# Kernel optimization log

Measured on AMD Instinct MI355X. Metric: run time of the kernel, lower is better.

The kernel has to match this reference:

```python
import jax, jax.numpy as jnp
import numpy as np

N = 100000   # nodes
E = 640000   # edges
DIN = 128
DOUT = 128
BN_EPS = 1e-5


def setup_inputs() -> dict:
    key = jax.random.key(0)
    k = jax.random.split(key, 6)
    x = jax.random.normal(k[0], (N, DIN), dtype=jnp.float32)
    edge_index = jax.random.randint(k[1], (2, E), 0, N, dtype=jnp.int64)
    # MLP params: Linear(DIN,DOUT) -> BatchNorm1d(DOUT) -> ReLU -> Linear(DOUT,DOUT)
    s1 = 1.0 / np.sqrt(DIN)
    s2 = 1.0 / np.sqrt(DOUT)
    W1 = jax.random.uniform(k[2], (DIN, DOUT), jnp.float32, -s1, s1)
    b1 = jax.random.uniform(k[3], (DOUT,), jnp.float32, -s1, s1)
    gamma = jnp.ones((DOUT,), jnp.float32)
    beta = jnp.zeros((DOUT,), jnp.float32)
    W2 = jax.random.uniform(k[4], (DOUT, DOUT), jnp.float32, -s2, s2)
    b2 = jax.random.uniform(k[5], (DOUT,), jnp.float32, -s2, s2)
    eps = jnp.zeros((), jnp.float32)  # train_eps=True, init 0.0
    return {"x": x, "edge_index": edge_index, "W1": W1, "b1": b1,
            "gamma": gamma, "beta": beta, "W2": W2, "b2": b2, "eps": eps}


def reference(x, edge_index, W1, b1, gamma, beta, W2, b2, eps):
    src = edge_index[0]
    dst = edge_index[1]
    # GIN sum aggregation: gather source features, scatter-add to target nodes
    agg = jax.ops.segment_sum(x[src], dst, num_segments=N)  # [N, DIN]
    h = agg + (1.0 + eps) * x  # eps-weighted residual combine
    # MLP: Linear -> BatchNorm1d (training stats, biased var) -> ReLU -> Linear
    h = h @ W1 + b1  # [N, DOUT]
    mu = jnp.mean(h, axis=0)
    var = jnp.mean((h - mu) ** 2, axis=0)
    h = (h - mu) * jax.lax.rsqrt(var + BN_EPS) * gamma + beta
    h = jnp.maximum(h, 0.0)
    return h @ W2 + b2
```

## Files before the change

### kernel.cpp

```cpp
#include <hip/hip_runtime.h>

#define N_NODES 100000
#define DIM     128
#define NEDGE   640000
#define BN_EPS  1e-5f

#define PB_CNT  2500
#define PB_X    6250
#define PB_W    64

#define NSLOT   32
#define NBUCKET 64
#define T_TILES 4
#define GGRID   1563
#define AGRID   6250

typedef __bf16 bf16x8 __attribute__((ext_vector_type(8)));
typedef float  f32x4  __attribute__((ext_vector_type(4)));
typedef unsigned short u16x8 __attribute__((ext_vector_type(8)));

__device__ __forceinline__ unsigned short f2b(float f) {
    unsigned u = __builtin_bit_cast(unsigned, f);
    u += 0x7fffu + ((u >> 16) & 1u);
    return (unsigned short)(u >> 16);
}
__device__ __forceinline__ float b2f(unsigned short b) {
    return __builtin_bit_cast(float, ((unsigned)b) << 16);
}

__global__ __launch_bounds__(256) void k_prep(const float* __restrict__ x,
                                              const float* __restrict__ W1,
                                              const float* __restrict__ W2,
                                              const int* __restrict__ ei,
                                              unsigned short* __restrict__ xb,
                                              unsigned short* __restrict__ Wt1,
                                              unsigned short* __restrict__ Wt2,
                                              unsigned* __restrict__ slots) {
    const int b = blockIdx.x;
    const int t = threadIdx.x;
    if (b < PB_CNT) {
        int e = b * 256 + t;
        unsigned src = (unsigned)ei[e];
        int dst = ei[NEDGE + e];
        unsigned* sp = slots + (size_t)dst * NSLOT;
        unsigned h = (unsigned)e;
        #pragma unroll 1
        for (int i = 0; i < NSLOT; ++i) {
            unsigned s = (h + (unsigned)i) & (NSLOT - 1);
            unsigned old = atomicCAS(&sp[s], 0xFFFFFFFFu, src);
            if (old == 0xFFFFFFFFu) break;
        }
    } else if (b < PB_CNT + PB_X) {
        size_t base = ((size_t)(b - PB_CNT) * 256 + t) * 8;
        float4 v0 = *(const float4*)(x + base);
        float4 v1 = *(const float4*)(x + base + 4);
        u16x8 o;
        o[0] = f2b(v0.x); o[1] = f2b(v0.y); o[2] = f2b(v0.z); o[3] = f2b(v0.w);
        o[4] = f2b(v1.x); o[5] = f2b(v1.y); o[6] = f2b(v1.z); o[7] = f2b(v1.w);
        *(u16x8*)(xb + base) = o;
    } else if (b < PB_CNT + PB_X + PB_W) {
        int idx = (b - PB_CNT - PB_X) * 256 + t;
        int k = idx >> 7, n = idx & 127;
        Wt1[n * 128 + k] = f2b(W1[idx]);
    } else {
        int idx = (b - PB_CNT - PB_X - PB_W) * 256 + t;
        int k = idx >> 7, n = idx & 127;
        Wt2[n * 128 + k] = f2b(W2[idx]);
    }
}

__global__ __launch_bounds__(256) void k_agg1(const unsigned short* __restrict__ xb,
                                              const unsigned* __restrict__ slots,
                                              const float* __restrict__ epsp,
                                              const unsigned short* __restrict__ Wt,
                                              const float* __restrict__ b1,
                                              unsigned short* __restrict__ hB,
                                              float* __restrict__ buckets) {
    __shared__ __align__(16) unsigned short At[16 * 136];
    __shared__ __align__(16) unsigned short stage[4][512];
    const int t = threadIdx.x;
    const int w = t >> 6;
    const int lane = t & 63;
    const int n15 = lane & 15;
    const int quad = lane >> 4;
    const int c8 = n15 * 8;
    const int gbase = lane & 48;

    const int row0 = blockIdx.x * 16;
    const int node = row0 + w * 4 + quad;

    int4 Bfr[2][4];
    const unsigned short* wp = Wt + (w * 32 + n15) * 128 + quad * 8;
    #pragma unroll
    for (int c = 0; c < 2; ++c)
        #pragma unroll
        for (int ks = 0; ks < 4; ++ks)
            Bfr[c][ks] = *(const int4*)(wp + c * 16 * 128 + ks * 32);
    float bias[2] = { b1[w * 32 + n15], b1[w * 32 + 16 + n15] };
    const float scale = 1.0f + epsp[0];

    const unsigned s_lo = slots[(size_t)node * NSLOT + n15];
    const unsigned s_hi = slots[(size_t)node * NSLOT + 16 + n15];
    float acc[8];
    {
        u16x8 v = *(const u16x8*)(xb + (size_t)node * 128 + c8);
        #pragma unroll
        for (int j = 0; j < 8; ++j) acc[j] = scale * b2f(v[j]);
    }
    unsigned long long blo = __ballot(s_lo != 0xFFFFFFFFu);
    unsigned long long bhi = __ballot(s_hi != 0xFFFFFFFFu);
    unsigned m = (unsigned)((blo >> gbase) & 0xFFFFull) |
                 ((unsigned)((bhi >> gbase) & 0xFFFFull) << 16);
    const int navail = __popc(m);
    unsigned mm = m;
    int pk = 0;
    for (int done = 0; done < navail; done += 8) {
        int4 va[8];
        #pragma unroll
        for (int k = 0; k < 8; ++k) {
            if (mm) { pk = (int)__builtin_ctz(mm); mm &= (mm - 1); }
            unsigned vlo = __shfl(s_lo, gbase + (pk & 15));
            unsigned vhi = __shfl(s_hi, gbase + (pk & 15));
            unsigned srck = (pk & 16) ? vhi : vlo;
            va[k] = *(const int4*)(xb + (size_t)srck * 128 + c8);
        }
        const int rem = navail - done;
        #pragma unroll
        for (int k = 0; k < 8; ++k) {
            if (k < rem) {
                u16x8 v = __builtin_bit_cast(u16x8, va[k]);
                #pragma unroll
                for (int j = 0; j < 8; ++j) acc[j] += b2f(v[j]);
            }
        }
    }
    {
        u16x8 o;
        #pragma unroll
        for (int j = 0; j < 8; ++j) o[j] = f2b(acc[j]);
        *(u16x8*)(At + (w * 4 + quad) * 136 + c8) = o;
    }
    __syncthreads();

    f32x4 accm[2] = {};
    #pragma unroll
    for (int ks = 0; ks < 4; ++ks) {
        int4 araw = *(const int4*)(At + n15 * 136 + ks * 32 + quad * 8);
        bf16x8 af = __builtin_bit_cast(bf16x8, araw);
        #pragma unroll
        for (int c = 0; c < 2; ++c)
            accm[c] = __builtin_amdgcn_mfma_f32_16x16x32_bf16(
                af, __builtin_bit_cast(bf16x8, Bfr[c][ks]), accm[c], 0, 0, 0);
    }
    float s[2] = {0.f, 0.f}, q[2] = {0.f, 0.f};
    unsigned short* st = stage[w];
    #pragma unroll
    for (int c = 0; c < 2; ++c)
        #pragma unroll
        for (int r = 0; r < 4; ++r) {
            float v = accm[c][r] + bias[c];
            s[c] += v; q[c] += v * v;
            st[(quad * 4 + r) * 32 + c * 16 + n15] = f2b(v);
        }
    {
        int so = lane * 8;
        int r = so >> 5, cc = so & 31;
        *(int4*)(hB + (size_t)(row0 + r) * 128 + w * 32 + cc) = *(const int4*)(st + so);
    }

    #pragma unroll
    for (int c = 0; c < 2; ++c) {
        s[c] += __shfl_down(s[c], 32); q[c] += __shfl_down(q[c], 32);
        s[c] += __shfl_down(s[c], 16); q[c] += __shfl_down(q[c], 16);
    }
    if (quad == 0) {
        float* bk = buckets + (blockIdx.x & (NBUCKET - 1)) * 256;
        atomicAdd(&bk[w * 32 + n15], s[0]);
        atomicAdd(&bk[w * 32 + 16 + n15], s[1]);
        atomicAdd(&bk[128 + w * 32 + n15], q[0]);
        atomicAdd(&bk[128 + w * 32 + 16 + n15], q[1]);
    }
}

__global__ void k_finalize(const float* __restrict__ gamma,
                           const float* __restrict__ beta,
                           const float* __restrict__ buckets,
                           float* __restrict__ aff) {
    int c = threadIdx.x;
    if (c < DIM) {
        float s = 0.f, q = 0.f;
        #pragma unroll 8
        for (int b = 0; b < NBUCKET; ++b) {
            s += buckets[b * 256 + c];
            q += buckets[b * 256 + 128 + c];
        }
        float mu  = s * (1.0f / N_NODES);
        float var = q * (1.0f / N_NODES) - mu * mu;
        float a = gamma[c] * rsqrtf(var + BN_EPS);
        aff[c] = a;
        aff[DIM + c] = beta[c] - mu * a;
    }
}

__global__ __launch_bounds__(256) void k_gemm2(const unsigned short* __restrict__ hb,
                                               const unsigned short* __restrict__ Wt2,
                                               const float* __restrict__ aff,
                                               const float* __restrict__ b2,
                                               float* __restrict__ out) {
    __shared__ __align__(16) unsigned short Asb[2][16 * 136];
    __shared__ __align__(16) float stage[4][512];
    const int t = threadIdx.x;
    const int w = t >> 6;
    const int lane = t & 63;
    const int n15 = lane & 15;
    const int quad = lane >> 4;
    const int c8 = n15 * 8;
    const int lrow = w * 4 + quad;

    int4 Bfr[2][4];
    const unsigned short* wp = Wt2 + (w * 32 + n15) * 128 + quad * 8;
    #pragma unroll
    for (int c = 0; c < 2; ++c)
        #pragma unroll
        for (int ks = 0; ks < 4; ++ks)
            Bfr[c][ks] = *(const int4*)(wp + c * 16 * 128 + ks * 32);

    float akr[8], bkr[8];
    *(float4*)(akr)     = *(const float4*)(aff + c8);
    *(float4*)(akr + 4) = *(const float4*)(aff + c8 + 4);
    *(float4*)(bkr)     = *(const float4*)(aff + 128 + c8);
    *(float4*)(bkr + 4) = *(const float4*)(aff + 128 + c8 + 4);
    float bias[2] = { b2[w * 32 + n15], b2[w * 32 + 16 + n15] };

    const int tile0 = blockIdx.x * T_TILES;
    float* st = stage[w];

    #pragma unroll
    for (int i = 0; i < T_TILES; ++i) {
        const int row0 = (tile0 + i) * 16;
        const bool valid = row0 < N_NODES;
        unsigned short* al = Asb[i & 1];
        if (valid) {
            int4 graw = *(const int4*)(hb + (size_t)(row0 + lrow) * 128 + c8);
            u16x8 ar = __builtin_bit_cast(u16x8, graw);
            u16x8 pr;
            #pragma unroll
            for (int j = 0; j < 8; ++j)
                pr[j] = f2b(fmaxf(fmaf(b2f(ar[j]), akr[j], bkr[j]), 0.f));
            *(int4*)(al + lrow * 136 + c8) = __builtin_bit_cast(int4, pr);
        }
        __syncthreads();
        if (valid) {
            f32x4 acc[2] = {};
            #pragma unroll
            for (int ks = 0; ks < 4; ++ks) {
                int4 araw = *(const int4*)(al + n15 * 136 + ks * 32 + quad * 8);
                bf16x8 af = __builtin_bit_cast(bf16x8, araw);
                #pragma unroll
                for (int c = 0; c < 2; ++c)
                    acc[c] = __builtin_amdgcn_mfma_f32_16x16x32_bf16(
                        af, __builtin_bit_cast(bf16x8, Bfr[c][ks]), acc[c], 0, 0, 0);
            }
            #pragma unroll
            for (int c = 0; c < 2; ++c)
                #pragma unroll
                for (int r = 0; r < 4; ++r)
                    st[(quad * 4 + r) * 32 + c * 16 + n15] = acc[c][r] + bias[c];
            #pragma unroll
            for (int p = 0; p < 2; ++p) {
                int fo = p * 256 + lane * 4;
                int r = fo >> 5, cc = fo & 31;
                *(float4*)(out + (size_t)(row0 + r) * 128 + w * 32 + cc) =
                    *(const float4*)(st + fo);
            }
        }
    }
}

extern "C" void kernel_launch(void* const* d_in, const int* in_sizes, int n_in,
                              void* d_out, int out_size, void* d_ws, size_t ws_size,
                              hipStream_t stream) {
    const float* x     = (const float*)d_in[0];
    const int*   ei    = (const int*)d_in[1];
    const float* W1    = (const float*)d_in[2];
    const float* b1    = (const float*)d_in[3];
    const float* gamma = (const float*)d_in[4];
    const float* beta  = (const float*)d_in[5];
    const float* W2    = (const float*)d_in[6];
    const float* b2    = (const float*)d_in[7];
    const float* eps   = (const float*)d_in[8];
    float* out = (float*)d_out;

    float* buckets      = (float*)d_ws;
    float* aff          = (float*)(buckets + NBUCKET * 256);
    unsigned short* hB  = (unsigned short*)(aff + 256);
    unsigned short* xb  = hB + (size_t)N_NODES * DIM;
    unsigned short* Wt1 = xb + (size_t)N_NODES * DIM;
    unsigned short* Wt2 = Wt1 + 16384;
    unsigned* slots     = (unsigned*)(Wt2 + 16384);

    hipMemsetAsync(buckets, 0, NBUCKET * 256 * sizeof(float), stream);
    hipMemsetAsync(slots, 0xFF, (size_t)N_NODES * NSLOT * sizeof(unsigned), stream);

    k_prep<<<PB_CNT + PB_X + 2 * PB_W, 256, 0, stream>>>(x, W1, W2, ei, xb, Wt1, Wt2,
                                                         slots);
    k_agg1<<<AGRID, 256, 0, stream>>>(xb, slots, eps, Wt1, b1, hB, buckets);
    k_finalize<<<1, 128, 0, stream>>>(gamma, beta, buckets, aff);
    k_gemm2<<<GGRID, 256, 0, stream>>>(hB, Wt2, aff, b2, out);
}
```

Baseline: 206.3 us.

## Merge memsets, fuse BN finalize into aggregation via last-block ticket, prefetch gemm2 rows

Result: slower. 433.3 us (+110.0%).

```diff
diff --git a/kernel.cpp b/kernel.cpp
--- a/kernel.cpp
+++ b/kernel.cpp
@@ -40,15 +40,15 @@
     const int t = threadIdx.x;
     if (b < PB_CNT) {
         int e = b * 256 + t;
-        unsigned src = (unsigned)ei[e];
+        unsigned srcp1 = (unsigned)ei[e] + 1u;
         int dst = ei[NEDGE + e];
         unsigned* sp = slots + (size_t)dst * NSLOT;
         unsigned h = (unsigned)e;
         #pragma unroll 1
         for (int i = 0; i < NSLOT; ++i) {
             unsigned s = (h + (unsigned)i) & (NSLOT - 1);
-            unsigned old = atomicCAS(&sp[s], 0xFFFFFFFFu, src);
-            if (old == 0xFFFFFFFFu) break;
+            unsigned old = atomicCAS(&sp[s], 0u, srcp1);
+            if (old == 0u) break;
         }
     } else if (b < PB_CNT + PB_X) {
         size_t base = ((size_t)(b - PB_CNT) * 256 + t) * 8;
@@ -75,9 +75,14 @@
                                               const unsigned short* __restrict__ Wt,
                                               const float* __restrict__ b1,
                                               unsigned short* __restrict__ hB,
-                                              float* __restrict__ buckets) {
+                                              float* __restrict__ buckets,
+                                              unsigned* __restrict__ ticket,
+                                              const float* __restrict__ gamma,
+                                              const float* __restrict__ beta,
+                                              float* __restrict__ aff) {
     __shared__ __align__(16) unsigned short At[16 * 136];
     __shared__ __align__(16) unsigned short stage[4][512];
+    __shared__ unsigned winner_s;
     const int t = threadIdx.x;
     const int w = t >> 6;
     const int lane = t & 63;
@@ -107,8 +112,8 @@
         #pragma unroll
         for (int j = 0; j < 8; ++j) acc[j] = scale * b2f(v[j]);
     }
-    unsigned long long blo = __ballot(s_lo != 0xFFFFFFFFu);
-    unsigned long long bhi = __ballot(s_hi != 0xFFFFFFFFu);
+    unsigned long long blo = __ballot(s_lo != 0u);
+    unsigned long long bhi = __ballot(s_hi != 0u);
     unsigned m = (unsigned)((blo >> gbase) & 0xFFFFull) |
                  ((unsigned)((bhi >> gbase) & 0xFFFFull) << 16);
     const int navail = __popc(m);
@@ -121,7 +126,7 @@
             if (mm) { pk = (int)__builtin_ctz(mm); mm &= (mm - 1); }
             unsigned vlo = __shfl(s_lo, gbase + (pk & 15));
             unsigned vhi = __shfl(s_hi, gbase + (pk & 15));
-            unsigned srck = (pk & 16) ? vhi : vlo;
+            unsigned srck = ((pk & 16) ? vhi : vlo) - 1u;
             va[k] = *(const int4*)(xb + (size_t)srck * 128 + c8);
         }
         const int rem = navail - done;
@@ -180,25 +185,26 @@
         atomicAdd(&bk[128 + w * 32 + n15], q[0]);
         atomicAdd(&bk[128 + w * 32 + 16 + n15], q[1]);
     }
-}
-
-__global__ void k_finalize(const float* __restrict__ gamma,
-                           const float* __restrict__ beta,
-                           const float* __restrict__ buckets,
-                           float* __restrict__ aff) {
-    int c = threadIdx.x;
-    if (c < DIM) {
-        float s = 0.f, q = 0.f;
+
+    __syncthreads();
+    if (t == 0) {
+        __threadfence();
+        winner_s = (atomicAdd(ticket, 1u) == AGRID - 1) ? 1u : 0u;
+    }
+    __syncthreads();
+    if (winner_s && t < 128) {
+        const volatile float* bk = (const volatile float*)buckets;
+        float ss = 0.f, qq = 0.f;
         #pragma unroll 8
         for (int b = 0; b < NBUCKET; ++b) {
-            s += buckets[b * 256 + c];
-            q += buckets[b * 256 + 128 + c];
-        }
-        float mu  = s * (1.0f / N_NODES);
-        float var = q * (1.0f / N_NODES) - mu * mu;
-        float a = gamma[c] * rsqrtf(var + BN_EPS);
-        aff[c] = a;
-        aff[DIM + c] = beta[c] - mu * a;
+            ss += bk[b * 256 + t];
+            qq += bk[b * 256 + 128 + t];
+        }
+        float mu  = ss * (1.0f / N_NODES);
+        float var = qq * (1.0f / N_NODES) - mu * mu;
+        float a = gamma[t] * rsqrtf(var + BN_EPS);
+        aff[t] = a;
+        aff[DIM + t] = beta[t] - mu * a;
     }
 }
 
@@ -233,6 +239,12 @@
     float bias[2] = { b2[w * 32 + n15], b2[w * 32 + 16 + n15] };
 
     const int tile0 = blockIdx.x * T_TILES;
+    int4 gr;
+    {
+        int r0 = tile0 * 16;
+        if (r0 < N_NODES)
+            gr = *(const int4*)(hb + (size_t)(r0 + lrow) * 128 + c8);
+    }
     float* st = stage[w];
 
     #pragma unroll
@@ -241,13 +253,17 @@
         const bool valid = row0 < N_NODES;
         unsigned short* al = Asb[i & 1];
         if (valid) {
-            int4 graw = *(const int4*)(hb + (size_t)(row0 + lrow) * 128 + c8);
-            u16x8 ar = __builtin_bit_cast(u16x8, graw);
+            u16x8 ar = __builtin_bit_cast(u16x8, gr);
             u16x8 pr;
             #pragma unroll
             for (int j = 0; j < 8; ++j)
                 pr[j] = f2b(fmaxf(fmaf(b2f(ar[j]), akr[j], bkr[j]), 0.f));
             *(int4*)(al + lrow * 136 + c8) = __builtin_bit_cast(int4, pr);
+        }
+        if (i + 1 < T_TILES) {
+            int rn = (tile0 + i + 1) * 16;
+            if (rn < N_NODES)
+                gr = *(const int4*)(hb + (size_t)(rn + lrow) * 128 + c8);
         }
         __syncthreads();
         if (valid) {
@@ -292,19 +308,21 @@
     float* out = (float*)d_out;
 
     float* buckets      = (float*)d_ws;
-    float* aff          = (float*)(buckets + NBUCKET * 256);
+    unsigned* ticket    = (unsigned*)(buckets + NBUCKET * 256);
+    unsigned* slots     = ticket + 64;
+    float* aff          = (float*)(slots + (size_t)N_NODES * NSLOT);
     unsigned short* hB  = (unsigned short*)(aff + 256);
     unsigned short* xb  = hB + (size_t)N_NODES * DIM;
     unsigned short* Wt1 = xb + (size_t)N_NODES * DIM;
     unsigned short* Wt2 = Wt1 + 16384;
-    unsigned* slots     = (unsigned*)(Wt2 + 16384);
-
-    hipMemsetAsync(buckets, 0, NBUCKET * 256 * sizeof(float), stream);
-    hipMemsetAsync(slots, 0xFF, (size_t)N_NODES * NSLOT * sizeof(unsigned), stream);
+
+    hipMemsetAsync(buckets, 0,
+                   NBUCKET * 256 * sizeof(float) + 64 * sizeof(unsigned) +
+                   (size_t)N_NODES * NSLOT * sizeof(unsigned), stream);
 
     k_prep<<<PB_CNT + PB_X + 2 * PB_W, 256, 0, stream>>>(x, W1, W2, ei, xb, Wt1, Wt2,
                                                          slots);
-    k_agg1<<<AGRID, 256, 0, stream>>>(xb, slots, eps, Wt1, b1, hB, buckets);
-    k_finalize<<<1, 128, 0, stream>>>(gamma, beta, buckets, aff);
+    k_agg1<<<AGRID, 256, 0, stream>>>(xb, slots, eps, Wt1, b1, hB, buckets,
+                                      ticket, gamma, beta, aff);
     k_gemm2<<<GGRID, 256, 0, stream>>>(hB, Wt2, aff, b2, out);
 }
```
